# Kernel tuning notes

Measured on AMD Instinct MI355X. Metric: run time of the kernel, lower is better.

The kernel has to match this reference:

```python
import jax, jax.numpy as jnp
import numpy as np

# Geometry constants replicating odl.tomo.parallel_beam_geometry for a
# 128x128 image on [-20,20]^2 (dx = 40/128 = 0.3125).
N_IMG = 128
EXTENT = 40.0
DX = EXTENT / N_IMG                      # 0.3125
RHO = 20.0 * np.sqrt(2.0)                # max corner radius ~= 28.284
N_ANG = 285                              # ceil(omega * rho), omega = pi/DX
N_DET = 183                              # 2*ceil(rho*omega/pi) + 1
N_T = 384                                # samples along each ray (~dx/1.2 step)
DT = 2.0 * RHO / N_T                     # integration step


def _sample_index_coords():
    """Pixel-index coordinates of all ray sample points.

    Returns float32 array [2, N_ANG, N_DET, N_T]: fractional indices into the
    image for bilinear interpolation. Rays for angle theta travel along
    d = (cos t, sin t); the detector axis is u = (-sin t, cos t).
    """
    ang = (np.arange(N_ANG) + 0.5) * np.pi / N_ANG          # cell centers on [0, pi)
    s = -RHO + (np.arange(N_DET) + 0.5) * (2.0 * RHO / N_DET)
    t = -RHO + (np.arange(N_T) + 0.5) * DT
    cos = np.cos(ang)[:, None, None]
    sin = np.sin(ang)[:, None, None]
    ss = s[None, :, None]
    tt = t[None, None, :]
    px = -ss * sin + tt * cos                               # physical x
    py = ss * cos + tt * sin                                # physical y
    i0 = (px + 20.0) / DX - 0.5                             # fractional row index
    i1 = (py + 20.0) / DX - 0.5                             # fractional col index
    return jnp.asarray(np.stack([i0, i1]), dtype=jnp.float32)


_COORDS = _sample_index_coords()


def setup_inputs() -> dict:
    key = jax.random.key(0)
    x = jax.random.normal(key, (8, N_IMG, N_IMG), dtype=jnp.float32)
    return {"x": x}


def reference(x):
    """Parallel-beam Radon forward projection of x/12 -> sinogram [B, 285, 183]."""
    xs = x / 12.0

    def project_one(img):
        # Bilinear gather at every (angle, det, ray-sample) point, zero outside.
        vals = jax.scipy.ndimage.map_coordinates(
            img, [_COORDS[0], _COORDS[1]], order=1, mode='constant', cval=0.0)
        # Line integral: sum along the ray * step size.
        return vals.sum(axis=-1) * DT                        # [N_ANG, N_DET]

    return jax.vmap(project_one)(xs)
```

## Files before the change

### kernel.cpp

```cpp
#include <hip/hip_runtime.h>
#include <stdint.h>

#define NI 128
#define NA 285
#define ND 183
#define NT 384
#define RAYS (NA * ND)
#define PITCH 133
#define PROWS 132
#define PLDS (PROWS * PITCH + 1)
#define TPB 832
#define NTASK 828
#define IDXM 17420
#define BIDXM (IDXM * 4)

typedef __fp16 half2v __attribute__((ext_vector_type(2)));

constexpr float PI_F  = 3.14159265358979323846f;
constexpr float RHO_F = 28.284271247461902f;
constexpr float DX_F  = 0.3125f;
constexpr float DT_F  = 2.0f * RHO_F / NT;

__global__ __launch_bounds__(TPB) void radon_fwd(const float* __restrict__ x,
                                                 float* __restrict__ out) {
    __shared__ __align__(16) unsigned int P[PLDS];
    const int tid   = threadIdx.x;
    const int img   = blockIdx.x >> 6;
    const int chunk = blockIdx.x & 63;

    for (int i = tid; i < 1432; i += TPB) {
        int r, c;
        if (i < 399) { r = (i < 133) ? 0 : (i < 266 ? 130 : 131);
                       c = i - ((i < 133) ? 0 : (i < 266 ? 133 : 266)); }
        else { int k = i - 399; r = 1 + (k >> 3);
               const int map[8] = {0, 1, 130, 131, 132, 0, 1, 130};
               c = map[k & 7]; }
        P[r * PITCH + c] = 0;
    }
    if (tid == 0) P[PLDS - 1] = 0;

    const float4* src = (const float4*)(x + img * NI * NI);
    for (int i = tid; i < 129 * 32; i += TPB) {
        int pr  = 1 + (i >> 5);
        int g   = i & 31;
        int rlo = pr - 2;
        int rhi = pr - 1;
        float4 vlo = (rlo >= 0)   ? src[rlo * 32 + g] : make_float4(0, 0, 0, 0);
        float4 vhi = (rhi <= 127) ? src[rhi * 32 + g] : make_float4(0, 0, 0, 0);
        int base = pr * PITCH + 2 + g * 4;
        P[base + 0] = __builtin_bit_cast(unsigned int, __builtin_amdgcn_cvt_pkrtz(vlo.x, vhi.x));
        P[base + 1] = __builtin_bit_cast(unsigned int, __builtin_amdgcn_cvt_pkrtz(vlo.y, vhi.y));
        P[base + 2] = __builtin_bit_cast(unsigned int, __builtin_amdgcn_cvt_pkrtz(vlo.z, vhi.z));
        P[base + 3] = __builtin_bit_cast(unsigned int, __builtin_amdgcn_cvt_pkrtz(vlo.w, vhi.w));
    }
    __syncthreads();

    const int w_id = tid >> 6;
    const int lane = tid & 63;
    const int t    = w_id * 64 + chunk;
    const int j    = t / 9;
    const int apc  = t - j * 9;
    const int ap   = apc * 16 + (lane >> 2);
    const int q    = lane & 3;
    const bool valid = (t < NTASK) && (ap < 143);

    const float ang = ((float)ap + 0.5f) * (PI_F / (float)NA);
    float sn, cs;
    sincosf(ang, &sn, &cs);
    const float s   = -RHO_F + ((float)j + 0.5f) * (2.0f * RHO_F / (float)ND);
    const float t0v = -RHO_F + 0.5f * DT_F;
    const float inv_dx = 1.0f / DX_F;

    const float e0 = -s * sn;
    const float e1 =  s * cs;
    const float c0p = (e0 + t0v * cs + 20.0f) * inv_dx + 1.5f;
    const float c1p = (e1 + t0v * sn + 20.0f) * inv_dx + 1.5f;
    const float st0 = DT_F * cs * inv_dx;
    const float st1 = DT_F * sn * inv_dx;

    const float LIM = 20.157f;
    const float inv_cs = 1.0f / cs;
    const float inv_sn = 1.0f / sn;
    float ta = (-LIM - e0) * inv_cs, tb = (LIM - e0) * inv_cs;
    float tc = (-LIM - e1) * inv_sn, td = (LIM - e1) * inv_sn;
    float tlo = fmaxf(fminf(ta, tb), fminf(tc, td));
    float thi = fminf(fmaxf(ta, tb), fmaxf(tc, td));

    const float inv_dt = 1.0f / DT_F;
    float fk0 = fminf(fmaxf(ceilf((tlo - t0v) * inv_dt), 0.0f), 384.0f);
    float fk1 = fminf(fmaxf(floorf((thi - t0v) * inv_dt), -1.0f), 383.0f);
    const int kmin = (int)fk0;
    const int kmax = (int)fk1;
    const int kmid = (kmin + kmax + 1) >> 1;

    int ldown = kmid - kmin;
    int lup   = kmax - kmid + 1;
    int mylen = (max(max(ldown, lup), 0) + 1) >> 1;
    if (!valid) mylen = 0;

    int Lw = mylen;
    #pragma unroll
    for (int off = 32; off >= 1; off >>= 1)
        Lw = max(Lw, __shfl_xor(Lw, off, 64));

    const int h = q >> 1;
    const int p = q & 1;
    const float sgn  = h ? 1.0f : -1.0f;
    const float st0s = st0 * (2.0f * sgn);
    const float st1s = st1 * (2.0f * sgn);
    const int   ks   = h ? (kmid + p) : (kmid - 1 - p);
    float i0 = fmaf((float)ks, st0, c0p);
    float i1 = fmaf((float)ks, st1, c1p);

    const char* Pb = (const char*)P;
    float acc0 = 0.0f, acc1 = 0.0f, acc2 = 0.0f, acc3 = 0.0f;

    #pragma unroll 4
    for (int m = 0; m < Lw; ++m) {
        float q0 = fminf(fmaxf(i0, 0.5f), 130.49f);
        float q1 = fminf(fmaxf(i1, 0.5f), 130.49f);
        i0 += st0s;
        i1 += st1s;
        float f0 = floorf(q0);
        float f1 = floorf(q1);
        float a0 = q0 - f0;
        float a1 = q1 - f1;
        float f1b = 4.0f * f1;
        int bidx  = (int)fmaf(f0, 532.0f, f1b);
        int bidx1 = BIDXM - bidx;
        int bidx2 = (int)fmaf(f0, 532.0f, 520.0f - f1b);
        int bidx3 = BIDXM - bidx2;
        unsigned int u0 = *(const unsigned int*)(Pb + bidx);
        unsigned int u1 = *(const unsigned int*)(Pb + bidx + 4);
        unsigned int m0 = *(const unsigned int*)(Pb + bidx1);
        unsigned int m1 = *(const unsigned int*)(Pb + bidx1 + 4);
        unsigned int r0 = *(const unsigned int*)(Pb + bidx2);
        unsigned int r1 = *(const unsigned int*)(Pb + bidx2 + 4);
        unsigned int s0 = *(const unsigned int*)(Pb + bidx3);
        unsigned int s1 = *(const unsigned int*)(Pb + bidx3 + 4);
        half2v w  = __builtin_amdgcn_cvt_pkrtz(1.0f - a0, a0);
        half2v b1 = __builtin_amdgcn_cvt_pkrtz(a1, a1);
        half2v wB = w * b1;
        half2v wA = w - wB;
        unsigned int wAu = __builtin_bit_cast(unsigned int, wA);
        unsigned int wBu = __builtin_bit_cast(unsigned int, wB);
        half2v wmA = __builtin_bit_cast(half2v, __builtin_amdgcn_alignbit(wAu, wAu, 16));
        half2v wmB = __builtin_bit_cast(half2v, __builtin_amdgcn_alignbit(wBu, wBu, 16));
        acc0 = __builtin_amdgcn_fdot2(__builtin_bit_cast(half2v, u0), wA, acc0, false);
        acc0 = __builtin_amdgcn_fdot2(__builtin_bit_cast(half2v, u1), wB, acc0, false);
        acc1 = __builtin_amdgcn_fdot2(__builtin_bit_cast(half2v, m0), wmB, acc1, false);
        acc1 = __builtin_amdgcn_fdot2(__builtin_bit_cast(half2v, m1), wmA, acc1, false);
        acc2 = __builtin_amdgcn_fdot2(__builtin_bit_cast(half2v, r0), wB, acc2, false);
        acc2 = __builtin_amdgcn_fdot2(__builtin_bit_cast(half2v, r1), wA, acc2, false);
        acc3 = __builtin_amdgcn_fdot2(__builtin_bit_cast(half2v, s0), wmA, acc3, false);
        acc3 = __builtin_amdgcn_fdot2(__builtin_bit_cast(half2v, s1), wmB, acc3, false);
    }

    acc0 += __shfl_xor(acc0, 1, 64); acc0 += __shfl_xor(acc0, 2, 64);
    acc1 += __shfl_xor(acc1, 1, 64); acc1 += __shfl_xor(acc1, 2, 64);
    acc2 += __shfl_xor(acc2, 1, 64); acc2 += __shfl_xor(acc2, 2, 64);
    acc3 += __shfl_xor(acc3, 1, 64); acc3 += __shfl_xor(acc3, 2, 64);

    if (valid) {
        float v = (q == 0) ? acc0 : (q == 1) ? acc1 : (q == 2) ? acc2 : acc3;
        int ao  = (q & 2) ? (284 - ap) : ap;
        int det = (q & 1) ? (182 - j) : j;
        out[img * RAYS + ao * ND + det] = v * (DT_F / 12.0f);
    }
}

extern "C" void kernel_launch(void* const* d_in, const int* in_sizes, int n_in,
                              void* d_out, int out_size, void* d_ws, size_t ws_size,
                              hipStream_t stream) {
    const float* x = (const float*)d_in[0];
    float* out = (float*)d_out;
    const int B = in_sizes[0] / (NI * NI);
    dim3 grid(B * 64);
    radon_fwd<<<grid, TPB, 0, stream>>>(x, out);
}
```

Baseline: 82.08 us.

## Drop four-way ray symmetry; assign per-angle detector groups with permuted round scheduling

The previous kernel handled four symmetric rays per lane: mirrored angle and detector indices reused one set of bilinear weights across four LDS gathers. The new version removes that symmetry and gives each wave a 16-detector group at a single angle. The four lanes per ray split the ray's samples, and tasks are spread over up to five rounds through a permuted slot index to balance load. The aim is better load balance and fewer wasted iterations, since the wave-wide max ray length is now taken over rays of one angle. The cost is repeated per-ray setup (sincos, clipping), losing the weight reuse across four rays, and more loop iterations in total.

```diff
diff --git a/kernel.cpp b/kernel.cpp
--- a/kernel.cpp
+++ b/kernel.cpp
@@ -10,9 +10,12 @@
 #define PROWS 132
 #define PLDS (PROWS * PITCH + 1)
 #define TPB 832
-#define NTASK 828
-#define IDXM 17420
-#define BIDXM (IDXM * 4)
+#define WAVES 13
+#define NBLK 64
+#define SLOTS (NBLK * WAVES)
+#define NGRP 12
+#define NTASKS (NA * NGRP)
+#define ROUNDS 5
 
 typedef __fp16 half2v __attribute__((ext_vector_type(2)));
 
@@ -24,9 +27,9 @@
 __global__ __launch_bounds__(TPB) void radon_fwd(const float* __restrict__ x,
                                                  float* __restrict__ out) {
     __shared__ __align__(16) unsigned int P[PLDS];
-    const int tid   = threadIdx.x;
-    const int img   = blockIdx.x >> 6;
-    const int chunk = blockIdx.x & 63;
+    const int tid = threadIdx.x;
+    const int img = blockIdx.x >> 6;
+    const int blk = blockIdx.x & 63;
 
     for (int i = tid; i < 1432; i += TPB) {
         int r, c;
@@ -57,115 +60,94 @@
 
     const int w_id = tid >> 6;
     const int lane = tid & 63;
-    const int t    = w_id * 64 + chunk;
-    const int j    = t / 9;
-    const int apc  = t - j * 9;
-    const int ap   = apc * 16 + (lane >> 2);
-    const int q    = lane & 3;
-    const bool valid = (t < NTASK) && (ap < 143);
-
-    const float ang = ((float)ap + 0.5f) * (PI_F / (float)NA);
-    float sn, cs;
-    sincosf(ang, &sn, &cs);
-    const float s   = -RHO_F + ((float)j + 0.5f) * (2.0f * RHO_F / (float)ND);
-    const float t0v = -RHO_F + 0.5f * DT_F;
-    const float inv_dx = 1.0f / DX_F;
-
-    const float e0 = -s * sn;
-    const float e1 =  s * cs;
-    const float c0p = (e0 + t0v * cs + 20.0f) * inv_dx + 1.5f;
-    const float c1p = (e1 + t0v * sn + 20.0f) * inv_dx + 1.5f;
-    const float st0 = DT_F * cs * inv_dx;
-    const float st1 = DT_F * sn * inv_dx;
-
-    const float LIM = 20.157f;
-    const float inv_cs = 1.0f / cs;
-    const float inv_sn = 1.0f / sn;
-    float ta = (-LIM - e0) * inv_cs, tb = (LIM - e0) * inv_cs;
-    float tc = (-LIM - e1) * inv_sn, td = (LIM - e1) * inv_sn;
-    float tlo = fmaxf(fminf(ta, tb), fminf(tc, td));
-    float thi = fminf(fmaxf(ta, tb), fmaxf(tc, td));
-
-    const float inv_dt = 1.0f / DT_F;
-    float fk0 = fminf(fmaxf(ceilf((tlo - t0v) * inv_dt), 0.0f), 384.0f);
-    float fk1 = fminf(fmaxf(floorf((thi - t0v) * inv_dt), -1.0f), 383.0f);
-    const int kmin = (int)fk0;
-    const int kmax = (int)fk1;
-    const int kmid = (kmin + kmax + 1) >> 1;
-
-    int ldown = kmid - kmin;
-    int lup   = kmax - kmid + 1;
-    int mylen = (max(max(ldown, lup), 0) + 1) >> 1;
-    if (!valid) mylen = 0;
-
-    int Lw = mylen;
-    #pragma unroll
-    for (int off = 32; off >= 1; off >>= 1)
-        Lw = max(Lw, __shfl_xor(Lw, off, 64));
-
-    const int h = q >> 1;
-    const int p = q & 1;
-    const float sgn  = h ? 1.0f : -1.0f;
-    const float st0s = st0 * (2.0f * sgn);
-    const float st1s = st1 * (2.0f * sgn);
-    const int   ks   = h ? (kmid + p) : (kmid - 1 - p);
-    float i0 = fmaf((float)ks, st0, c0p);
-    float i1 = fmaf((float)ks, st1, c1p);
+    const int sidx = blk * WAVES + w_id;
+    const int perm = (sidx * 181) % SLOTS;
+    const int dloc = lane & 15;
+    const int q    = lane >> 4;
+    const int h    = q >> 1;
+    const int pp   = q & 1;
+    const float sgn = h ? 1.0f : -1.0f;
 
     const char* Pb = (const char*)P;
-    float acc0 = 0.0f, acc1 = 0.0f, acc2 = 0.0f, acc3 = 0.0f;
+    const float inv_dx = 1.0f / DX_F;
+    const float inv_dt = 1.0f / DT_F;
+    const float t0v    = -RHO_F + 0.5f * DT_F;
+    const float LIM    = 20.157f;
 
-    #pragma unroll 4
-    for (int m = 0; m < Lw; ++m) {
-        float q0 = fminf(fmaxf(i0, 0.5f), 130.49f);
-        float q1 = fminf(fmaxf(i1, 0.5f), 130.49f);
-        i0 += st0s;
-        i1 += st1s;
-        float f0 = floorf(q0);
-        float f1 = floorf(q1);
-        float a0 = q0 - f0;
-        float a1 = q1 - f1;
-        float f1b = 4.0f * f1;
-        int bidx  = (int)fmaf(f0, 532.0f, f1b);
-        int bidx1 = BIDXM - bidx;
-        int bidx2 = (int)fmaf(f0, 532.0f, 520.0f - f1b);
-        int bidx3 = BIDXM - bidx2;
-        unsigned int u0 = *(const unsigned int*)(Pb + bidx);
-        unsigned int u1 = *(const unsigned int*)(Pb + bidx + 4);
-        unsigned int m0 = *(const unsigned int*)(Pb + bidx1);
-        unsigned int m1 = *(const unsigned int*)(Pb + bidx1 + 4);
-        unsigned int r0 = *(const unsigned int*)(Pb + bidx2);
-        unsigned int r1 = *(const unsigned int*)(Pb + bidx2 + 4);
-        unsigned int s0 = *(const unsigned int*)(Pb + bidx3);
-        unsigned int s1 = *(const unsigned int*)(Pb + bidx3 + 4);
-        half2v w  = __builtin_amdgcn_cvt_pkrtz(1.0f - a0, a0);
-        half2v b1 = __builtin_amdgcn_cvt_pkrtz(a1, a1);
-        half2v wB = w * b1;
-        half2v wA = w - wB;
-        unsigned int wAu = __builtin_bit_cast(unsigned int, wA);
-        unsigned int wBu = __builtin_bit_cast(unsigned int, wB);
-        half2v wmA = __builtin_bit_cast(half2v, __builtin_amdgcn_alignbit(wAu, wAu, 16));
-        half2v wmB = __builtin_bit_cast(half2v, __builtin_amdgcn_alignbit(wBu, wBu, 16));
-        acc0 = __builtin_amdgcn_fdot2(__builtin_bit_cast(half2v, u0), wA, acc0, false);
-        acc0 = __builtin_amdgcn_fdot2(__builtin_bit_cast(half2v, u1), wB, acc0, false);
-        acc1 = __builtin_amdgcn_fdot2(__builtin_bit_cast(half2v, m0), wmB, acc1, false);
-        acc1 = __builtin_amdgcn_fdot2(__builtin_bit_cast(half2v, m1), wmA, acc1, false);
-        acc2 = __builtin_amdgcn_fdot2(__builtin_bit_cast(half2v, r0), wB, acc2, false);
-        acc2 = __builtin_amdgcn_fdot2(__builtin_bit_cast(half2v, r1), wA, acc2, false);
-        acc3 = __builtin_amdgcn_fdot2(__builtin_bit_cast(half2v, s0), wmA, acc3, false);
-        acc3 = __builtin_amdgcn_fdot2(__builtin_bit_cast(half2v, s1), wmB, acc3, false);
-    }
+    for (int r = 0; r < ROUNDS; ++r) {
+        const int task = r * SLOTS + perm;
+        if (task >= NTASKS) break;
+        const int a = task / NGRP;
+        const int g = task - a * NGRP;
+        const int d = g * 16 + dloc;
+        const bool valid = (d < ND);
 
-    acc0 += __shfl_xor(acc0, 1, 64); acc0 += __shfl_xor(acc0, 2, 64);
-    acc1 += __shfl_xor(acc1, 1, 64); acc1 += __shfl_xor(acc1, 2, 64);
-    acc2 += __shfl_xor(acc2, 1, 64); acc2 += __shfl_xor(acc2, 2, 64);
-    acc3 += __shfl_xor(acc3, 1, 64); acc3 += __shfl_xor(acc3, 2, 64);
+        const float ang = ((float)a + 0.5f) * (PI_F / (float)NA);
+        float sn, cs;
+        sincosf(ang, &sn, &cs);
+        const float s = -RHO_F + ((float)d + 0.5f) * (2.0f * RHO_F / (float)ND);
 
-    if (valid) {
-        float v = (q == 0) ? acc0 : (q == 1) ? acc1 : (q == 2) ? acc2 : acc3;
-        int ao  = (q & 2) ? (284 - ap) : ap;
-        int det = (q & 1) ? (182 - j) : j;
-        out[img * RAYS + ao * ND + det] = v * (DT_F / 12.0f);
+        const float e0 = -s * sn;
+        const float e1 =  s * cs;
+        const float c0p = (e0 + t0v * cs + 20.0f) * inv_dx + 1.5f;
+        const float c1p = (e1 + t0v * sn + 20.0f) * inv_dx + 1.5f;
+        const float st0 = DT_F * cs * inv_dx;
+        const float st1 = DT_F * sn * inv_dx;
+
+        const float inv_cs = 1.0f / cs;
+        const float inv_sn = 1.0f / sn;
+        float ta = (-LIM - e0) * inv_cs, tb = (LIM - e0) * inv_cs;
+        float tc = (-LIM - e1) * inv_sn, td = (LIM - e1) * inv_sn;
+        float tlo = fmaxf(fminf(ta, tb), fminf(tc, td));
+        float thi = fminf(fmaxf(ta, tb), fmaxf(tc, td));
+        float fk0 = fminf(fmaxf(ceilf((tlo - t0v) * inv_dt), 0.0f), 384.0f);
+        float fk1 = fminf(fmaxf(floorf((thi - t0v) * inv_dt), -1.0f), 383.0f);
+        const int kmin = (int)fk0;
+        const int kmax = (int)fk1;
+        const int kmid = (kmin + kmax + 1) >> 1;
+
+        int ldown = kmid - kmin;
+        int lup   = kmax - kmid + 1;
+        int mylen = (max(max(ldown, lup), 0) + 1) >> 1;
+        if (!valid) mylen = 0;
+
+        int Lw = mylen;
+        #pragma unroll
+        for (int off = 32; off >= 1; off >>= 1)
+            Lw = max(Lw, __shfl_xor(Lw, off, 64));
+
+        const float st0s = st0 * (2.0f * sgn);
+        const float st1s = st1 * (2.0f * sgn);
+        const int   ks   = h ? (kmid + pp) : (kmid - 1 - pp);
+        float i0 = fmaf((float)ks, st0, c0p);
+        float i1 = fmaf((float)ks, st1, c1p);
+        float acc = 0.0f;
+
+        #pragma unroll 4
+        for (int m = 0; m < Lw; ++m) {
+            float q0 = fminf(fmaxf(i0, 0.5f), 130.49f);
+            float q1 = fminf(fmaxf(i1, 0.5f), 130.49f);
+            i0 += st0s;
+            i1 += st1s;
+            float f0 = floorf(q0);
+            float f1 = floorf(q1);
+            float a0 = q0 - f0;
+            float a1 = q1 - f1;
+            int bidx = (int)fmaf(f0, 532.0f, 4.0f * f1);
+            unsigned int u0 = *(const unsigned int*)(Pb + bidx);
+            unsigned int u1 = *(const unsigned int*)(Pb + bidx + 4);
+            half2v w  = __builtin_amdgcn_cvt_pkrtz(1.0f - a0, a0);
+            half2v b1 = __builtin_amdgcn_cvt_pkrtz(a1, a1);
+            half2v wB = w * b1;
+            half2v wA = w - wB;
+            acc = __builtin_amdgcn_fdot2(__builtin_bit_cast(half2v, u0), wA, acc, false);
+            acc = __builtin_amdgcn_fdot2(__builtin_bit_cast(half2v, u1), wB, acc, false);
+        }
+
+        acc += __shfl_xor(acc, 16, 64);
+        acc += __shfl_xor(acc, 32, 64);
+        if (valid && q == 0)
+            out[img * RAYS + a * ND + d] = acc * (DT_F / 12.0f);
     }
 }
 
@@ -175,6 +157,6 @@
     const float* x = (const float*)d_in[0];
     float* out = (float*)d_out;
     const int B = in_sizes[0] / (NI * NI);
-    dim3 grid(B * 64);
+    dim3 grid(B * NBLK);
     radon_fwd<<<grid, TPB, 0, stream>>>(x, out);
 }
```

Measured after the change: 119.2 us. 45.2% more time.

## Remap wave tasks to one angle by sixteen detectors with permuted round-robin scheduling

Applied to the files above, without the earlier changes.

Each wave now handles a single angle with 16 consecutive detector offsets, and the four symmetric quarter-samples sit across lane groups instead of adjacent lanes. Tasks (143 angles x 6 detector groups) are spread over waves through a multiplicative permutation and processed in up to two rounds per wave. The intent is to keep ray lengths within a wave more uniform, so the max-length loop wastes fewer iterations, and to balance work across blocks. The cost is a second round for some waves, plus repeated sincos and bounds setup per task.

```diff
diff --git a/kernel.cpp b/kernel.cpp
--- a/kernel.cpp
+++ b/kernel.cpp
@@ -10,7 +10,13 @@
 #define PROWS 132
 #define PLDS (PROWS * PITCH + 1)
 #define TPB 832
-#define NTASK 828
+#define WAVES 13
+#define NBLK 64
+#define SLOTS (NBLK * WAVES)
+#define NAP 143
+#define NGRPJ 6
+#define NTASKS (NAP * NGRPJ)
+#define ROUNDS 2
 #define IDXM 17420
 #define BIDXM (IDXM * 4)
 
@@ -24,9 +30,9 @@
 __global__ __launch_bounds__(TPB) void radon_fwd(const float* __restrict__ x,
                                                  float* __restrict__ out) {
     __shared__ __align__(16) unsigned int P[PLDS];
-    const int tid   = threadIdx.x;
-    const int img   = blockIdx.x >> 6;
-    const int chunk = blockIdx.x & 63;
+    const int tid = threadIdx.x;
+    const int img = blockIdx.x >> 6;
+    const int blk = blockIdx.x & 63;
 
     for (int i = tid; i < 1432; i += TPB) {
         int r, c;
@@ -57,115 +63,121 @@
 
     const int w_id = tid >> 6;
     const int lane = tid & 63;
-    const int t    = w_id * 64 + chunk;
-    const int j    = t / 9;
-    const int apc  = t - j * 9;
-    const int ap   = apc * 16 + (lane >> 2);
-    const int q    = lane & 3;
-    const bool valid = (t < NTASK) && (ap < 143);
-
-    const float ang = ((float)ap + 0.5f) * (PI_F / (float)NA);
-    float sn, cs;
-    sincosf(ang, &sn, &cs);
-    const float s   = -RHO_F + ((float)j + 0.5f) * (2.0f * RHO_F / (float)ND);
-    const float t0v = -RHO_F + 0.5f * DT_F;
-    const float inv_dx = 1.0f / DX_F;
-
-    const float e0 = -s * sn;
-    const float e1 =  s * cs;
-    const float c0p = (e0 + t0v * cs + 20.0f) * inv_dx + 1.5f;
-    const float c1p = (e1 + t0v * sn + 20.0f) * inv_dx + 1.5f;
-    const float st0 = DT_F * cs * inv_dx;
-    const float st1 = DT_F * sn * inv_dx;
-
-    const float LIM = 20.157f;
-    const float inv_cs = 1.0f / cs;
-    const float inv_sn = 1.0f / sn;
-    float ta = (-LIM - e0) * inv_cs, tb = (LIM - e0) * inv_cs;
-    float tc = (-LIM - e1) * inv_sn, td = (LIM - e1) * inv_sn;
-    float tlo = fmaxf(fminf(ta, tb), fminf(tc, td));
-    float thi = fminf(fmaxf(ta, tb), fmaxf(tc, td));
-
-    const float inv_dt = 1.0f / DT_F;
-    float fk0 = fminf(fmaxf(ceilf((tlo - t0v) * inv_dt), 0.0f), 384.0f);
-    float fk1 = fminf(fmaxf(floorf((thi - t0v) * inv_dt), -1.0f), 383.0f);
-    const int kmin = (int)fk0;
-    const int kmax = (int)fk1;
-    const int kmid = (kmin + kmax + 1) >> 1;
-
-    int ldown = kmid - kmin;
-    int lup   = kmax - kmid + 1;
-    int mylen = (max(max(ldown, lup), 0) + 1) >> 1;
-    if (!valid) mylen = 0;
-
-    int Lw = mylen;
-    #pragma unroll
-    for (int off = 32; off >= 1; off >>= 1)
-        Lw = max(Lw, __shfl_xor(Lw, off, 64));
-
-    const int h = q >> 1;
-    const int p = q & 1;
-    const float sgn  = h ? 1.0f : -1.0f;
-    const float st0s = st0 * (2.0f * sgn);
-    const float st1s = st1 * (2.0f * sgn);
-    const int   ks   = h ? (kmid + p) : (kmid - 1 - p);
-    float i0 = fmaf((float)ks, st0, c0p);
-    float i1 = fmaf((float)ks, st1, c1p);
+    const int sidx = blk * WAVES + w_id;
+    const int perm = (sidx * 181) % SLOTS;
+    const int dloc = lane & 15;
+    const int q    = lane >> 4;
+    const int h    = q >> 1;
+    const int pp   = q & 1;
+    const float sgn = h ? 1.0f : -1.0f;
 
     const char* Pb = (const char*)P;
-    float acc0 = 0.0f, acc1 = 0.0f, acc2 = 0.0f, acc3 = 0.0f;
+    const float inv_dx = 1.0f / DX_F;
+    const float inv_dt = 1.0f / DT_F;
+    const float t0v    = -RHO_F + 0.5f * DT_F;
+    const float LIM    = 20.157f;
 
-    #pragma unroll 4
-    for (int m = 0; m < Lw; ++m) {
-        float q0 = fminf(fmaxf(i0, 0.5f), 130.49f);
-        float q1 = fminf(fmaxf(i1, 0.5f), 130.49f);
-        i0 += st0s;
-        i1 += st1s;
-        float f0 = floorf(q0);
-        float f1 = floorf(q1);
-        float a0 = q0 - f0;
-        float a1 = q1 - f1;
-        float f1b = 4.0f * f1;
-        int bidx  = (int)fmaf(f0, 532.0f, f1b);
-        int bidx1 = BIDXM - bidx;
-        int bidx2 = (int)fmaf(f0, 532.0f, 520.0f - f1b);
-        int bidx3 = BIDXM - bidx2;
-        unsigned int u0 = *(const unsigned int*)(Pb + bidx);
-        unsigned int u1 = *(const unsigned int*)(Pb + bidx + 4);
-        unsigned int m0 = *(const unsigned int*)(Pb + bidx1);
-        unsigned int m1 = *(const unsigned int*)(Pb + bidx1 + 4);
-        unsigned int r0 = *(const unsigned int*)(Pb + bidx2);
-        unsigned int r1 = *(const unsigned int*)(Pb + bidx2 + 4);
-        unsigned int s0 = *(const unsigned int*)(Pb + bidx3);
-        unsigned int s1 = *(const unsigned int*)(Pb + bidx3 + 4);
-        half2v w  = __builtin_amdgcn_cvt_pkrtz(1.0f - a0, a0);
-        half2v b1 = __builtin_amdgcn_cvt_pkrtz(a1, a1);
-        half2v wB = w * b1;
-        half2v wA = w - wB;
-        unsigned int wAu = __builtin_bit_cast(unsigned int, wA);
-        unsigned int wBu = __builtin_bit_cast(unsigned int, wB);
-        half2v wmA = __builtin_bit_cast(half2v, __builtin_amdgcn_alignbit(wAu, wAu, 16));
-        half2v wmB = __builtin_bit_cast(half2v, __builtin_amdgcn_alignbit(wBu, wBu, 16));
-        acc0 = __builtin_amdgcn_fdot2(__builtin_bit_cast(half2v, u0), wA, acc0, false);
-        acc0 = __builtin_amdgcn_fdot2(__builtin_bit_cast(half2v, u1), wB, acc0, false);
-        acc1 = __builtin_amdgcn_fdot2(__builtin_bit_cast(half2v, m0), wmB, acc1, false);
-        acc1 = __builtin_amdgcn_fdot2(__builtin_bit_cast(half2v, m1), wmA, acc1, false);
-        acc2 = __builtin_amdgcn_fdot2(__builtin_bit_cast(half2v, r0), wB, acc2, false);
-        acc2 = __builtin_amdgcn_fdot2(__builtin_bit_cast(half2v, r1), wA, acc2, false);
-        acc3 = __builtin_amdgcn_fdot2(__builtin_bit_cast(half2v, s0), wmA, acc3, false);
-        acc3 = __builtin_amdgcn_fdot2(__builtin_bit_cast(half2v, s1), wmB, acc3, false);
-    }
+    for (int r = 0; r < ROUNDS; ++r) {
+        const int task = r * SLOTS + perm;
+        if (task >= NTASKS) break;
+        const int ap = task / NGRPJ;
+        const int g  = task - ap * NGRPJ;
+        const int j  = g * 16 + dloc;
+        const bool valid = (j < 92);
 
-    acc0 += __shfl_xor(acc0, 1, 64); acc0 += __shfl_xor(acc0, 2, 64);
-    acc1 += __shfl_xor(acc1, 1, 64); acc1 += __shfl_xor(acc1, 2, 64);
-    acc2 += __shfl_xor(acc2, 1, 64); acc2 += __shfl_xor(acc2, 2, 64);
-    acc3 += __shfl_xor(acc3, 1, 64); acc3 += __shfl_xor(acc3, 2, 64);
+        const float ang = ((float)ap + 0.5f) * (PI_F / (float)NA);
+        float sn, cs;
+        sincosf(ang, &sn, &cs);
+        const float s = -RHO_F + ((float)j + 0.5f) * (2.0f * RHO_F / (float)ND);
 
-    if (valid) {
-        float v = (q == 0) ? acc0 : (q == 1) ? acc1 : (q == 2) ? acc2 : acc3;
-        int ao  = (q & 2) ? (284 - ap) : ap;
-        int det = (q & 1) ? (182 - j) : j;
-        out[img * RAYS + ao * ND + det] = v * (DT_F / 12.0f);
+        const float e0 = -s * sn;
+        const float e1 =  s * cs;
+        const float c0p = (e0 + t0v * cs + 20.0f) * inv_dx + 1.5f;
+        const float c1p = (e1 + t0v * sn + 20.0f) * inv_dx + 1.5f;
+        const float st0 = DT_F * cs * inv_dx;
+        const float st1 = DT_F * sn * inv_dx;
+
+        const float inv_cs = 1.0f / cs;
+        const float inv_sn = 1.0f / sn;
+        float ta = (-LIM - e0) * inv_cs, tb = (LIM - e0) * inv_cs;
+        float tc = (-LIM - e1) * inv_sn, td = (LIM - e1) * inv_sn;
+        float tlo = fmaxf(fminf(ta, tb), fminf(tc, td));
+        float thi = fminf(fmaxf(ta, tb), fmaxf(tc, td));
+        float fk0 = fminf(fmaxf(ceilf((tlo - t0v) * inv_dt), 0.0f), 384.0f);
+        float fk1 = fminf(fmaxf(floorf((thi - t0v) * inv_dt), -1.0f), 383.0f);
+        const int kmin = (int)fk0;
+        const int kmax = (int)fk1;
+        const int kmid = (kmin + kmax + 1) >> 1;
+
+        int ldown = kmid - kmin;
+        int lup   = kmax - kmid + 1;
+        int mylen = (max(max(ldown, lup), 0) + 1) >> 1;
+        if (!valid) mylen = 0;
+
+        int Lw = mylen;
+        #pragma unroll
+        for (int off = 32; off >= 1; off >>= 1)
+            Lw = max(Lw, __shfl_xor(Lw, off, 64));
+
+        const float st0s = st0 * (2.0f * sgn);
+        const float st1s = st1 * (2.0f * sgn);
+        const int   ks   = h ? (kmid + pp) : (kmid - 1 - pp);
+        float i0 = fmaf((float)ks, st0, c0p);
+        float i1 = fmaf((float)ks, st1, c1p);
+        float acc0 = 0.0f, acc1 = 0.0f, acc2 = 0.0f, acc3 = 0.0f;
+
+        #pragma unroll 4
+        for (int m = 0; m < Lw; ++m) {
+            float q0 = fminf(fmaxf(i0, 0.5f), 130.49f);
+            float q1 = fminf(fmaxf(i1, 0.5f), 130.49f);
+            i0 += st0s;
+            i1 += st1s;
+            float f0 = floorf(q0);
+            float f1 = floorf(q1);
+            float a0 = q0 - f0;
+            float a1 = q1 - f1;
+            float f1b = 4.0f * f1;
+            int bidx  = (int)fmaf(f0, 532.0f, f1b);
+            int bidx1 = BIDXM - bidx;
+            int bidx2 = (int)fmaf(f0, 532.0f, 520.0f - f1b);
+            int bidx3 = BIDXM - bidx2;
+            unsigned int u0 = *(const unsigned int*)(Pb + bidx);
+            unsigned int u1 = *(const unsigned int*)(Pb + bidx + 4);
+            unsigned int m0 = *(const unsigned int*)(Pb + bidx1);
+            unsigned int m1 = *(const unsigned int*)(Pb + bidx1 + 4);
+            unsigned int r0 = *(const unsigned int*)(Pb + bidx2);
+            unsigned int r1 = *(const unsigned int*)(Pb + bidx2 + 4);
+            unsigned int s0 = *(const unsigned int*)(Pb + bidx3);
+            unsigned int s1 = *(const unsigned int*)(Pb + bidx3 + 4);
+            half2v w  = __builtin_amdgcn_cvt_pkrtz(1.0f - a0, a0);
+            half2v b1 = __builtin_amdgcn_cvt_pkrtz(a1, a1);
+            half2v wB = w * b1;
+            half2v wA = w - wB;
+            unsigned int wAu = __builtin_bit_cast(unsigned int, wA);
+            unsigned int wBu = __builtin_bit_cast(unsigned int, wB);
+            half2v wmA = __builtin_bit_cast(half2v, __builtin_amdgcn_alignbit(wAu, wAu, 16));
+            half2v wmB = __builtin_bit_cast(half2v, __builtin_amdgcn_alignbit(wBu, wBu, 16));
+            acc0 = __builtin_amdgcn_fdot2(__builtin_bit_cast(half2v, u0), wA, acc0, false);
+            acc0 = __builtin_amdgcn_fdot2(__builtin_bit_cast(half2v, u1), wB, acc0, false);
+            acc1 = __builtin_amdgcn_fdot2(__builtin_bit_cast(half2v, m0), wmB, acc1, false);
+            acc1 = __builtin_amdgcn_fdot2(__builtin_bit_cast(half2v, m1), wmA, acc1, false);
+            acc2 = __builtin_amdgcn_fdot2(__builtin_bit_cast(half2v, r0), wB, acc2, false);
+            acc2 = __builtin_amdgcn_fdot2(__builtin_bit_cast(half2v, r1), wA, acc2, false);
+            acc3 = __builtin_amdgcn_fdot2(__builtin_bit_cast(half2v, s0), wmA, acc3, false);
+            acc3 = __builtin_amdgcn_fdot2(__builtin_bit_cast(half2v, s1), wmB, acc3, false);
+        }
+
+        acc0 += __shfl_xor(acc0, 16, 64); acc0 += __shfl_xor(acc0, 32, 64);
+        acc1 += __shfl_xor(acc1, 16, 64); acc1 += __shfl_xor(acc1, 32, 64);
+        acc2 += __shfl_xor(acc2, 16, 64); acc2 += __shfl_xor(acc2, 32, 64);
+        acc3 += __shfl_xor(acc3, 16, 64); acc3 += __shfl_xor(acc3, 32, 64);
+
+        if (valid) {
+            float v = (q == 0) ? acc0 : (q == 1) ? acc1 : (q == 2) ? acc2 : acc3;
+            int ao  = (q & 2) ? (284 - ap) : ap;
+            int det = (q & 1) ? (182 - j) : j;
+            out[img * RAYS + ao * ND + det] = v * (DT_F / 12.0f);
+        }
     }
 }
 
@@ -175,6 +187,6 @@
     const float* x = (const float*)d_in[0];
     float* out = (float*)d_out;
     const int B = in_sizes[0] / (NI * NI);
-    dim3 grid(B * 64);
+    dim3 grid(B * NBLK);
     radon_fwd<<<grid, TPB, 0, stream>>>(x, out);
 }
```

New measurement: 94.71 us. 1.15x slower.
